# Kernel optimization log

Hardware: AMD Instinct MI355X
Metric: run time of the kernel (lower is better)

## Reference

```python
import jax, jax.numpy as jnp
import numpy as np

NUM_NODES = 40000
NUM_EDGES = 400000
DIM = 128
NUM_REL = 502  # num_relation * 2
NUM_HEAD = 1


def setup_inputs() -> dict:
    key = jax.random.key(0)
    ks = jax.random.split(key, 16)
    d = DIM
    return {
        "curr_stat": jax.random.normal(ks[0], (NUM_NODES, d), jnp.float32),
        "last_stat": jax.random.normal(ks[1], (NUM_NODES, d), jnp.float32),
        "relemb_weight": jax.random.normal(ks[2], (NUM_REL, d), jnp.float32),
        "selfrel_weight": jax.random.normal(ks[3], (1, d), jnp.float32),
        "Wq": jax.random.normal(ks[4], (2 * d, d), jnp.float32) * (1.0 / np.sqrt(2 * d)),
        "bq": jax.random.normal(ks[5], (d,), jnp.float32) * 0.02,
        "Wk": jax.random.normal(ks[6], (2 * d, d), jnp.float32) * (1.0 / np.sqrt(2 * d)),
        "bk": jax.random.normal(ks[7], (d,), jnp.float32) * 0.02,
        "Wv": jax.random.normal(ks[8], (d, d), jnp.float32) * (1.0 / np.sqrt(d)),
        "bv": jax.random.normal(ks[9], (d,), jnp.float32) * 0.02,
        "dyn_weight": jax.random.normal(ks[10], (d, d), jnp.float32) * (1.0 / np.sqrt(d)),
        "edge_index": jax.random.randint(ks[11], (2, NUM_EDGES), 0, NUM_NODES, jnp.int32),
        "edge_type": jax.random.randint(ks[12], (NUM_EDGES,), 0, NUM_REL, jnp.int32),
    }


def _segment_softmax(scores, seg, num_segments):
    # scores: [E, H]; softmax over edges sharing the same destination segment
    m = jax.ops.segment_max(scores, seg, num_segments=num_segments)  # [N, H]
    e = jnp.exp(scores - m[seg])
    s = jax.ops.segment_sum(e, seg, num_segments=num_segments)  # [N, H]
    return e / s[seg]


def reference(curr_stat, last_stat, relemb_weight, selfrel_weight,
              Wq, bq, Wk, bk, Wv, bv, dyn_weight,
              edge_index, edge_type):
    N, D = curr_stat.shape
    H = NUM_HEAD
    HD = D // H

    # append self-loop edges for every node, with the dedicated self-relation
    loop = jnp.arange(N, dtype=edge_index.dtype)
    src = jnp.concatenate([edge_index[0], loop])  # [E_total]
    dst = jnp.concatenate([edge_index[1], loop])  # [E_total]
    type_emb = jnp.concatenate(
        [relemb_weight[edge_type], jnp.broadcast_to(selfrel_weight, (N, D))], axis=0)

    E = src.shape[0]
    # linear projections (x @ W + b); torch Linear stores W transposed, same math
    q = (jnp.concatenate([curr_stat[dst], type_emb], -1) @ Wq + bq).reshape(E, H, HD)
    k = (jnp.concatenate([last_stat[src], type_emb], -1) @ Wk + bk).reshape(E, H, HD)
    v = (last_stat[src] @ Wv + bv).reshape(E, H, HD)

    attn = jnp.sum(q * k, axis=-1) / np.sqrt(HD).astype(np.float32)  # [E, H]

    dyn_prob = _segment_softmax(attn, dst, N)   # [E, H]
    sta_prob = _segment_softmax(-attn, dst, N)  # [E, H]

    counts = jax.ops.segment_sum(jnp.ones((E,), jnp.float32), dst, num_segments=N)
    denom = jnp.maximum(counts, 1.0)[:, None]  # scatter-mean denominator

    feat_dyn = jax.ops.segment_sum((dyn_prob[..., None] * v).reshape(E, D), dst,
                                   num_segments=N) / denom
    feat_sta = jax.ops.segment_sum((sta_prob[..., None] * v).reshape(E, D), dst,
                                   num_segments=N) / denom

    # stack (feat_sta, feat_dyn @ dyn_weight) -> [2, N, D]
    return jnp.stack([feat_sta, feat_dyn @ dyn_weight])
```

## Files before the change

kernel.cpp:

```cpp
#include <hip/hip_runtime.h>
#include <hip/hip_bf16.h>
#include <math.h>

#define DIMC 128

typedef __attribute__((ext_vector_type(8))) short short8;
typedef __attribute__((ext_vector_type(4))) float floatx4;
typedef __attribute__((ext_vector_type(2))) float f32x2;

static __device__ __forceinline__ unsigned pk2(float lo, float hi) {
    __hip_bfloat162 h = __float22bfloat162_rn(make_float2(lo, hi));
    return *(unsigned*)&h;
}
static __device__ __forceinline__ unsigned short f2bf(float x) {
    union { float f; unsigned int u; } v; v.f = x;
    unsigned int r = v.u + 0x7FFFu + ((v.u >> 16) & 1u);
    return (unsigned short)(r >> 16);
}
static __device__ __forceinline__ f32x2 bfp(unsigned int u) {
    union { unsigned int i; float f; } a, b;
    a.i = u << 16; b.i = u & 0xFFFF0000u;
    f32x2 r; r.x = a.f; r.y = b.f; return r;
}

template<int CTRL>
static __device__ __forceinline__ float dpp_add(float x) {
    int y = __builtin_amdgcn_update_dpp(0, __float_as_int(x), CTRL, 0xF, 0xF, true);
    return x + __int_as_float(y);
}
static __device__ __forceinline__ float red32(float p) {
    p = dpp_add<0xB1>(p);
    p = dpp_add<0x4E>(p);
    p = dpp_add<0x141>(p);
    p = dpp_add<0x140>(p);
    p += __shfl_xor(p, 16);
    return p;
}

struct PrepArgs {
    const float* W[6];
    unsigned short* F[6];
    const float* relemb; const float* selfrel;
    float* TypeEmb;
    int* deg;
    int R; int N;
};

__global__ __launch_bounds__(64) void prep_all(PrepArgs a)
{
    int b = blockIdx.x;
    int lane = threadIdx.x;
    if (b < 192) {
        int mat = b >> 5, ts = b & 31;
        int s = ts & 3, t = ts >> 2;
        int q = lane >> 4, c = lane & 15;
        const float* W = a.W[mat];
        unsigned short o[8];
        #pragma unroll
        for (int j = 0; j < 8; ++j)
            o[j] = f2bf(W[(long)(s * 32 + q * 8 + j) * DIMC + t * 16 + c]);
        uint4 u;
        u.x = (unsigned)o[0] | ((unsigned)o[1] << 16);
        u.y = (unsigned)o[2] | ((unsigned)o[3] << 16);
        u.z = (unsigned)o[4] | ((unsigned)o[5] << 16);
        u.w = (unsigned)o[6] | ((unsigned)o[7] << 16);
        ((uint4*)a.F[mat])[ts * 64 + lane] = u;
    } else if (b < 192 + a.R + 1) {
        int r = b - 192;
        const float* src = (r < a.R) ? (a.relemb + (long)r * DIMC) : a.selfrel;
        float2 v = ((const float2*)src)[lane];
        ((float2*)(a.TypeEmb + (long)r * DIMC))[lane] = v;
    } else {
        int i = (b - (192 + a.R + 1)) * 64 + lane;
        if (i < a.N) a.deg[i] = 0;
    }
}

struct GemmM5 {
    const float*          Af[5];
    const unsigned short* Ab[5];
    const unsigned short* F[5];
    const float*          bias[5];
    float*                outf[5];
    unsigned short*       outb[5];
    int                   ostride[5];
    int                   ooff[5];
    int                   M[5];
    const int*            hist_dst;
    int*                  hist_deg;
    int                   hist_E;
};

__global__ __launch_bounds__(256) void gemm_mfma(GemmM5 g)
{
    if (blockIdx.y == 5) {
        int i = blockIdx.x * blockDim.x + threadIdx.x;
        int stride = gridDim.x * blockDim.x;
        for (; i < g.hist_E; i += stride) atomicAdd(&g.hist_deg[g.hist_dst[i]], 1);
        return;
    }

    const int which = blockIdx.y;
    const int M = g.M[which];
    if (blockIdx.x * 64 >= M) return;

    const float*          __restrict__ Af   = g.Af[which];
    const unsigned short* __restrict__ Ab   = g.Ab[which];
    const unsigned short* __restrict__ F    = g.F[which];
    const float*          __restrict__ bias = g.bias[which];
    float*          __restrict__ outf = g.outf[which];
    unsigned short* __restrict__ outb = g.outb[which];
    const int ostride = g.ostride[which];
    const int ooff    = g.ooff[which];

    const int wave = threadIdx.x >> 6;
    const int lane = threadIdx.x & 63;
    const int q = lane >> 4, c = lane & 15;
    const int rowbase = blockIdx.x * 64 + wave * 16;

    short8 wf[8][4];
    const uint4* Fp = (const uint4*)F;
    #pragma unroll
    for (int t = 0; t < 8; ++t)
        #pragma unroll
        for (int s = 0; s < 4; ++s) {
            uint4 u = Fp[(t * 4 + s) * 64 + lane];
            wf[t][s] = *(short8*)&u;
        }

    floatx4 acc[8];
    #pragma unroll
    for (int t = 0; t < 8; ++t) {
        float b = bias ? bias[t * 16 + c] : 0.0f;
        acc[t] = (floatx4){b, b, b, b};
    }

    int rowA = rowbase + c; if (rowA > M - 1) rowA = M - 1;
    short8 af[4];
    if (Af) {
        const float* Ar = Af + (long)rowA * DIMC + q * 8;
        #pragma unroll
        for (int s = 0; s < 4; ++s) {
            float4 x0 = *(const float4*)(Ar + s * 32);
            float4 x1 = *(const float4*)(Ar + s * 32 + 4);
            uint4 u;
            u.x = pk2(x0.x, x0.y);
            u.y = pk2(x0.z, x0.w);
            u.z = pk2(x1.x, x1.y);
            u.w = pk2(x1.z, x1.w);
            af[s] = *(short8*)&u;
        }
    } else {
        const unsigned short* Ar = Ab + (long)rowA * DIMC + q * 8;
        #pragma unroll
        for (int s = 0; s < 4; ++s) {
            uint4 u = *(const uint4*)(Ar + s * 32);
            af[s] = *(short8*)&u;
        }
    }

    #pragma unroll
    for (int t = 0; t < 8; ++t)
        #pragma unroll
        for (int s = 0; s < 4; ++s)
            acc[t] = __builtin_amdgcn_mfma_f32_16x16x32_bf16(af[s], wf[t][s], acc[t], 0, 0, 0);

    if (outf) {
        #pragma unroll
        for (int t = 0; t < 8; ++t)
            #pragma unroll
            for (int r = 0; r < 4; ++r) {
                int row = rowbase + q * 4 + r;
                if (row < M)
                    outf[(long)row * DIMC + t * 16 + c] = acc[t][r];
            }
    } else {
        #pragma unroll
        for (int t = 0; t < 8; ++t)
            #pragma unroll
            for (int r = 0; r < 4; ++r) {
                float other = __shfl_xor(acc[t][r], 1);
                int row = rowbase + q * 4 + r;
                if ((lane & 1) == 0 && row < M) {
                    unsigned word = pk2(acc[t][r], other);
                    ((unsigned*)outb)[((long)row * 64 + t * 8 + (c >> 1))
                                      * (long)ostride + ooff] = word;
                }
            }
    }
}

__global__ __launch_bounds__(256) void partial_sums(const int* __restrict__ deg,
                                                    int* __restrict__ partial, int N)
{
    __shared__ int sh[256];
    int t = threadIdx.x;
    int beg = blockIdx.x * 1024 + t * 4;
    int s = 0;
    if (beg + 3 < N) { int4 v = *(const int4*)(deg + beg); s = v.x + v.y + v.z + v.w; }
    else { for (int j = 0; j < 4; ++j) if (beg + j < N) s += deg[beg + j]; }
    sh[t] = s;
    __syncthreads();
    for (int d = 128; d >= 1; d >>= 1) {
        if (t < d) sh[t] += sh[t + d];
        __syncthreads();
    }
    if (t == 0) partial[blockIdx.x] = sh[0];
}

__global__ __launch_bounds__(256) void scan_write_offsets(const int* __restrict__ deg,
                                                          const int* __restrict__ partial,
                                                          int* __restrict__ offs,
                                                          int* __restrict__ cursor, int N, int nb)
{
    __shared__ int sh[256];
    __shared__ int sbase;
    int t = threadIdx.x;
    if (t < 64) {
        int v = (t < nb && t < (int)blockIdx.x) ? partial[t] : 0;
        #pragma unroll
        for (int d = 32; d >= 1; d >>= 1) v += __shfl_xor(v, d);
        if (t == 0) sbase = v;
    }
    int beg = blockIdx.x * 1024 + t * 4;
    int d0 = 0, d1 = 0, d2 = 0, d3 = 0;
    if (beg + 3 < N) { int4 v = *(const int4*)(deg + beg); d0 = v.x; d1 = v.y; d2 = v.z; d3 = v.w; }
    else {
        if (beg < N)     d0 = deg[beg];
        if (beg + 1 < N) d1 = deg[beg + 1];
        if (beg + 2 < N) d2 = deg[beg + 2];
        if (beg + 3 < N) d3 = deg[beg + 3];
    }
    int s = d0 + d1 + d2 + d3;
    sh[t] = s;
    __syncthreads();
    for (int d = 1; d < 256; d <<= 1) {
        int v = (t >= d) ? sh[t - d] : 0;
        __syncthreads();
        sh[t] += v;
        __syncthreads();
    }
    int base = sbase + sh[t] - s;
    int o0 = base, o1 = o0 + d0, o2 = o1 + d1, o3 = o2 + d2;
    if (beg < N)     { offs[beg]     = o0; cursor[beg]     = o0; }
    if (beg + 1 < N) { offs[beg + 1] = o1; cursor[beg + 1] = o1; }
    if (beg + 2 < N) { offs[beg + 2] = o2; cursor[beg + 2] = o2; }
    if (beg + 3 < N) { offs[beg + 3] = o3; cursor[beg + 3] = o3; }
}

__global__ void scatter_kernel(const int* __restrict__ src, const int* __restrict__ dst,
                               const int* __restrict__ etype, int* __restrict__ cursor,
                               int2* __restrict__ sedge, int E)
{
    int e = blockIdx.x * blockDim.x + threadIdx.x;
    if (e < E) {
        int d = dst[e];
        int p = atomicAdd(&cursor[d], 1);
        sedge[p] = make_int2(src[e] << 8, etype[e] << 9);
    }
}

__global__ __launch_bounds__(256) void node_kernel(
    const float* __restrict__ Qn,
    const char*  __restrict__ Kb,
    const char*  __restrict__ Vb,
    const char*  __restrict__ QKb,
    const int* __restrict__ offs, const int* __restrict__ deg,
    const int2* __restrict__ sedge,
    float* __restrict__ out_sta, uint2* __restrict__ feat_dyn,
    int N, int R)
{
    int n = (blockIdx.x * blockDim.x + threadIdx.x) >> 6;
    int lane = threadIdx.x & 63;
    if (n >= N) return;
    const int hl = lane & 31;
    const int h  = lane >> 5;
    const int lo8  = hl << 3;
    const int lo16 = hl << 4;

    const float cs2 = 0.08838834764831845f * 1.4426950408889634f;
    int base = offs[n];
    int dcnt = deg[n];

    float4 qn4 = ((const float4*)(Qn + (long)n * DIMC))[hl];
    f32x2 q01; q01.x = qn4.x; q01.y = qn4.y;
    f32x2 q23; q23.x = qn4.z; q23.y = qn4.w;

    uint2 ks  = *(const uint2*)(Kb + ((long)n << 8) + lo8);
    uint2 vs  = *(const uint2*)(Vb + ((long)n << 8) + lo8);
    uint4 qks = *(const uint4*)(QKb + ((long)R << 9) + lo16);
    {
        f32x2 s0 = q01 + bfp(qks.x);
        f32x2 s1 = q23 + bfp(qks.z);
        f32x2 k0 = bfp(ks.x) + bfp(qks.y);
        f32x2 k1 = bfp(ks.y) + bfp(qks.w);
        f32x2 dp = s0 * k0;
        dp += s1 * k1;
        float p = red32(dp.x + dp.y);
        float t = p * cs2;
        float wd = (h == 0) ? exp2f(t)  : 0.0f;
        float ws = (h == 0) ? exp2f(-t) : 0.0f;
        f32x2 v0 = bfp(vs.x), v1 = bfp(vs.y);

        float s_d = wd, s_s = ws;
        f32x2 accd0 = v0 * wd, accd1 = v1 * wd;
        f32x2 accs0 = v0 * ws, accs1 = v1 * ws;

        int T = (dcnt + 3) >> 2;
        for (int it = 0; it < T; ++it) {
            int iA = 4 * it + 2 * h, iB = iA + 1;
            bool vA = iA < dcnt, vB = iB < dcnt;
            int2 eA = sedge[vA ? (base + iA) : 0];
            int2 eB = sedge[vB ? (base + iB) : 0];
            uint2 kA  = *(const uint2*)(Kb + eA.x + lo8);
            uint2 vAv = *(const uint2*)(Vb + eA.x + lo8);
            uint4 qkA = *(const uint4*)(QKb + eA.y + lo16);
            uint2 kB  = *(const uint2*)(Kb + eB.x + lo8);
            uint2 vBv = *(const uint2*)(Vb + eB.x + lo8);
            uint4 qkB = *(const uint4*)(QKb + eB.y + lo16);

            f32x2 a0 = q01 + bfp(qkA.x), a1 = q23 + bfp(qkA.z);
            f32x2 ka0 = bfp(kA.x) + bfp(qkA.y), ka1 = bfp(kA.y) + bfp(qkA.w);
            f32x2 da = a0 * ka0;
            da += a1 * ka1;
            float pA = da.x + da.y;

            f32x2 b0 = q01 + bfp(qkB.x), b1 = q23 + bfp(qkB.z);
            f32x2 kb0 = bfp(kB.x) + bfp(qkB.y), kb1 = bfp(kB.y) + bfp(qkB.w);
            f32x2 db = b0 * kb0;
            db += b1 * kb1;
            float pB = db.x + db.y;

            pA = red32(pA);
            pB = red32(pB);
            float tA = pA * cs2, tB = pB * cs2;

            float wdA = vA ? exp2f(tA)  : 0.0f;
            float wsA = vA ? exp2f(-tA) : 0.0f;
            float wdB = vB ? exp2f(tB)  : 0.0f;
            float wsB = vB ? exp2f(-tB) : 0.0f;

            s_d += wdA + wdB;
            s_s += wsA + wsB;

            f32x2 va0 = bfp(vAv.x), va1 = bfp(vAv.y);
            f32x2 vb0 = bfp(vBv.x), vb1 = bfp(vBv.y);
            accd0 += va0 * wdA;  accd0 += vb0 * wdB;
            accd1 += va1 * wdA;  accd1 += vb1 * wdB;
            accs0 += va0 * wsA;  accs0 += vb0 * wsB;
            accs1 += va1 * wsA;  accs1 += vb1 * wsB;
        }

        s_d += __shfl_xor(s_d, 32);
        s_s += __shfl_xor(s_s, 32);
        accd0.x += __shfl_xor(accd0.x, 32); accd0.y += __shfl_xor(accd0.y, 32);
        accd1.x += __shfl_xor(accd1.x, 32); accd1.y += __shfl_xor(accd1.y, 32);
        accs0.x += __shfl_xor(accs0.x, 32); accs0.y += __shfl_xor(accs0.y, 32);
        accs1.x += __shfl_xor(accs1.x, 32); accs1.y += __shfl_xor(accs1.y, 32);

        if (h == 0) {
            float denom = (float)(dcnt + 1);
            float id_ = 1.0f / (s_d * denom);
            float is_ = 1.0f / (s_s * denom);
            ((float4*)(out_sta + (long)n * DIMC))[hl] =
                make_float4(accs0.x * is_, accs0.y * is_, accs1.x * is_, accs1.y * is_);
            feat_dyn[(unsigned)n * 32u + hl] =
                make_uint2(pk2(accd0.x * id_, accd0.y * id_), pk2(accd1.x * id_, accd1.y * id_));
        }
    }
}

extern "C" void kernel_launch(void* const* d_in, const int* in_sizes, int n_in,
                              void* d_out, int out_size, void* d_ws, size_t ws_size,
                              hipStream_t stream)
{
    const float* curr    = (const float*)d_in[0];
    const float* last    = (const float*)d_in[1];
    const float* relemb  = (const float*)d_in[2];
    const float* selfrel = (const float*)d_in[3];
    const float* Wq      = (const float*)d_in[4];
    const float* bq      = (const float*)d_in[5];
    const float* Wk      = (const float*)d_in[6];
    const float* bk      = (const float*)d_in[7];
    const float* Wv      = (const float*)d_in[8];
    const float* bv      = (const float*)d_in[9];
    const float* dynw    = (const float*)d_in[10];
    const int*   eidx    = (const int*)d_in[11];
    const int*   etype   = (const int*)d_in[12];
    float* out = (float*)d_out;

    const int N = in_sizes[0] / DIMC;
    const int E = in_sizes[12];
    const int R = in_sizes[2] / DIMC;
    const int* esrc = eidx;
    const int* edst = eidx + E;

    char* wp = (char*)d_ws;
    auto alloc = [&](size_t bytes) { char* r = wp; wp += (bytes + 15) & ~(size_t)15; return r; };
    size_t nd = (size_t)N * DIMC;
    float*          Qn    = (float*)alloc(nd * 4);
    unsigned short* Kb    = (unsigned short*)alloc((size_t)N * 256);
    unsigned short* Vb    = (unsigned short*)alloc((size_t)N * 256);
    unsigned short* Fdb   = (unsigned short*)alloc(nd * 2);
    uint4*          QKre  = (uint4*)alloc((size_t)(R + 1) * 32 * 16);
    float*          TypeEmb = (float*)alloc((size_t)(R + 2) * DIMC * 4);
    unsigned short* FW[6];
    for (int m = 0; m < 6; ++m) FW[m] = (unsigned short*)alloc(2048 * 8 * 2);
    int*            deg   = (int*)alloc((size_t)N * 4);
    int*            offs  = (int*)alloc((size_t)N * 4);
    int*            cursor= (int*)alloc((size_t)N * 4);
    int2*           sedge = (int2*)alloc((size_t)E * 8);
    int*            partial = (int*)alloc(256 * 4);

    const int gblk = N / 64;
    const int sblk = (N + 1023) / 1024;

    PrepArgs pa;
    pa.W[0] = Wq;   pa.W[1] = Wk;   pa.W[2] = Wv;
    pa.W[3] = dynw; pa.W[4] = Wq + (size_t)DIMC * DIMC; pa.W[5] = Wk + (size_t)DIMC * DIMC;
    for (int m = 0; m < 6; ++m) pa.F[m] = FW[m];
    pa.relemb = relemb; pa.selfrel = selfrel; pa.TypeEmb = TypeEmb;
    pa.deg = deg; pa.R = R; pa.N = N;
    int pgrid = 192 + (R + 1) + (N + 63) / 64;
    hipLaunchKernelGGL(prep_all, dim3(pgrid), dim3(64), 0, stream, pa);

    GemmM5 g5;
    for (int s = 0; s < 5; ++s) { g5.Ab[s] = nullptr; g5.outf[s] = nullptr; g5.outb[s] = nullptr; }
    g5.Af[0] = curr;    g5.F[0] = FW[0]; g5.bias[0] = nullptr; g5.outf[0] = Qn;
    g5.ostride[0] = 1;  g5.ooff[0] = 0;  g5.M[0] = N;
    g5.Af[1] = last;    g5.F[1] = FW[1]; g5.bias[1] = nullptr; g5.outb[1] = Kb;
    g5.ostride[1] = 1;  g5.ooff[1] = 0;  g5.M[1] = N;
    g5.Af[2] = last;    g5.F[2] = FW[2]; g5.bias[2] = bv;      g5.outb[2] = Vb;
    g5.ostride[2] = 1;  g5.ooff[2] = 0;  g5.M[2] = N;
    g5.Af[3] = TypeEmb; g5.F[3] = FW[4]; g5.bias[3] = bq;      g5.outb[3] = (unsigned short*)QKre;
    g5.ostride[3] = 2;  g5.ooff[3] = 0;  g5.M[3] = R + 1;
    g5.Af[4] = TypeEmb; g5.F[4] = FW[5]; g5.bias[4] = bk;      g5.outb[4] = (unsigned short*)QKre;
    g5.ostride[4] = 2;  g5.ooff[4] = 1;  g5.M[4] = R + 1;
    g5.hist_dst = edst; g5.hist_deg = deg; g5.hist_E = E;
    hipLaunchKernelGGL(gemm_mfma, dim3(gblk, 6), dim3(256), 0, stream, g5);

    hipLaunchKernelGGL(partial_sums, dim3(sblk), dim3(256), 0, stream, deg, partial, N);
    hipLaunchKernelGGL(scan_write_offsets, dim3(sblk), dim3(256), 0, stream,
                       deg, partial, offs, cursor, N, sblk);
    hipLaunchKernelGGL(scatter_kernel, dim3((E + 255) / 256), dim3(256), 0, stream,
                       esrc, edst, etype, cursor, sedge, E);

    hipLaunchKernelGGL(node_kernel, dim3((N + 3) / 4), dim3(256), 0, stream,
                       Qn, (const char*)Kb, (const char*)Vb, (const char*)QKre,
                       offs, deg, sedge, out, (uint2*)Fdb, N, R);

    GemmM5 gf;
    for (int s = 0; s < 5; ++s) { gf.Af[s] = nullptr; gf.Ab[s] = nullptr; gf.outf[s] = nullptr; gf.outb[s] = nullptr; gf.M[s] = 0; }
    gf.Ab[0] = Fdb; gf.F[0] = FW[3]; gf.bias[0] = nullptr; gf.outf[0] = out + nd;
    gf.ostride[0] = 1; gf.ooff[0] = 0; gf.M[0] = N;
    gf.hist_dst = edst; gf.hist_deg = deg; gf.hist_E = 0;
    hipLaunchKernelGGL(gemm_mfma, dim3(gblk, 1), dim3(256), 0, stream, gf);
}
```

Before: 221.3 us.

## Software-pipeline edge gathers in node kernel and fold softmax scale into Q weights

The node kernel's edge loop is restructured into a two-stage software pipeline: edge indices for the next iteration and K/V/QK gathers for the current one are issued before the compute on the previous batch, which hides gather latency. The attention scale (1/sqrt(D)·log2e) is folded into the Wq weights and the q-side bias during prep, removing per-edge multiplies. The block size drops from 256 to 128 threads (2 nodes per block). The cost is higher register pressure from the double-buffered loads and bf16 rounding applied to scaled weights.

```diff
diff --git a/kernel.cpp b/kernel.cpp
--- a/kernel.cpp
+++ b/kernel.cpp
@@ -3,6 +3,7 @@
 #include <math.h>
 
 #define DIMC 128
+#define CS2L (0.08838834764831845f * 1.4426950408889634f)
 
 typedef __attribute__((ext_vector_type(8))) short short8;
 typedef __attribute__((ext_vector_type(4))) float floatx4;
@@ -40,6 +41,7 @@
 struct PrepArgs {
     const float* W[6];
     unsigned short* F[6];
+    float wscale[6];
     const float* relemb; const float* selfrel;
     float* TypeEmb;
     int* deg;
@@ -55,10 +57,11 @@
         int s = ts & 3, t = ts >> 2;
         int q = lane >> 4, c = lane & 15;
         const float* W = a.W[mat];
+        float sc = a.wscale[mat];
         unsigned short o[8];
         #pragma unroll
         for (int j = 0; j < 8; ++j)
-            o[j] = f2bf(W[(long)(s * 32 + q * 8 + j) * DIMC + t * 16 + c]);
+            o[j] = f2bf(W[(long)(s * 32 + q * 8 + j) * DIMC + t * 16 + c] * sc);
         uint4 u;
         u.x = (unsigned)o[0] | ((unsigned)o[1] << 16);
         u.y = (unsigned)o[2] | ((unsigned)o[3] << 16);
@@ -81,6 +84,7 @@
     const unsigned short* Ab[5];
     const unsigned short* F[5];
     const float*          bias[5];
+    float                 bscale[5];
     float*                outf[5];
     unsigned short*       outb[5];
     int                   ostride[5];
@@ -108,6 +112,7 @@
     const unsigned short* __restrict__ Ab   = g.Ab[which];
     const unsigned short* __restrict__ F    = g.F[which];
     const float*          __restrict__ bias = g.bias[which];
+    const float bsc = g.bscale[which];
     float*          __restrict__ outf = g.outf[which];
     unsigned short* __restrict__ outb = g.outb[which];
     const int ostride = g.ostride[which];
@@ -131,7 +136,7 @@
     floatx4 acc[8];
     #pragma unroll
     for (int t = 0; t < 8; ++t) {
-        float b = bias ? bias[t * 16 + c] : 0.0f;
+        float b = bias ? bias[t * 16 + c] * bsc : 0.0f;
         acc[t] = (floatx4){b, b, b, b};
     }
 
@@ -260,7 +265,7 @@
     }
 }
 
-__global__ __launch_bounds__(256) void node_kernel(
+__global__ __launch_bounds__(128) void node_kernel(
     const float* __restrict__ Qn,
     const char*  __restrict__ Kb,
     const char*  __restrict__ Vb,
@@ -270,7 +275,7 @@
     float* __restrict__ out_sta, uint2* __restrict__ feat_dyn,
     int N, int R)
 {
-    int n = (blockIdx.x * blockDim.x + threadIdx.x) >> 6;
+    int n = blockIdx.x * 2 + (threadIdx.x >> 6);
     int lane = threadIdx.x & 63;
     if (n >= N) return;
     const int hl = lane & 31;
@@ -278,7 +283,6 @@
     const int lo8  = hl << 3;
     const int lo16 = hl << 4;
 
-    const float cs2 = 0.08838834764831845f * 1.4426950408889634f;
     int base = offs[n];
     int dcnt = deg[n];
 
@@ -289,6 +293,9 @@
     uint2 ks  = *(const uint2*)(Kb + ((long)n << 8) + lo8);
     uint2 vs  = *(const uint2*)(Vb + ((long)n << 8) + lo8);
     uint4 qks = *(const uint4*)(QKb + ((long)R << 9) + lo16);
+
+    float s_d, s_s;
+    f32x2 accd0, accd1, accs0, accs1;
     {
         f32x2 s0 = q01 + bfp(qks.x);
         f32x2 s1 = q23 + bfp(qks.z);
@@ -296,77 +303,102 @@
         f32x2 k1 = bfp(ks.y) + bfp(qks.w);
         f32x2 dp = s0 * k0;
         dp += s1 * k1;
-        float p = red32(dp.x + dp.y);
-        float t = p * cs2;
+        float t = red32(dp.x + dp.y);
         float wd = (h == 0) ? exp2f(t)  : 0.0f;
         float ws = (h == 0) ? exp2f(-t) : 0.0f;
         f32x2 v0 = bfp(vs.x), v1 = bfp(vs.y);
-
-        float s_d = wd, s_s = ws;
-        f32x2 accd0 = v0 * wd, accd1 = v1 * wd;
-        f32x2 accs0 = v0 * ws, accs1 = v1 * ws;
-
-        int T = (dcnt + 3) >> 2;
-        for (int it = 0; it < T; ++it) {
-            int iA = 4 * it + 2 * h, iB = iA + 1;
-            bool vA = iA < dcnt, vB = iB < dcnt;
-            int2 eA = sedge[vA ? (base + iA) : 0];
-            int2 eB = sedge[vB ? (base + iB) : 0];
-            uint2 kA  = *(const uint2*)(Kb + eA.x + lo8);
-            uint2 vAv = *(const uint2*)(Vb + eA.x + lo8);
-            uint4 qkA = *(const uint4*)(QKb + eA.y + lo16);
-            uint2 kB  = *(const uint2*)(Kb + eB.x + lo8);
-            uint2 vBv = *(const uint2*)(Vb + eB.x + lo8);
-            uint4 qkB = *(const uint4*)(QKb + eB.y + lo16);
-
-            f32x2 a0 = q01 + bfp(qkA.x), a1 = q23 + bfp(qkA.z);
-            f32x2 ka0 = bfp(kA.x) + bfp(qkA.y), ka1 = bfp(kA.y) + bfp(qkA.w);
-            f32x2 da = a0 * ka0;
-            da += a1 * ka1;
-            float pA = da.x + da.y;
-
-            f32x2 b0 = q01 + bfp(qkB.x), b1 = q23 + bfp(qkB.z);
-            f32x2 kb0 = bfp(kB.x) + bfp(qkB.y), kb1 = bfp(kB.y) + bfp(qkB.w);
-            f32x2 db = b0 * kb0;
-            db += b1 * kb1;
-            float pB = db.x + db.y;
-
-            pA = red32(pA);
-            pB = red32(pB);
-            float tA = pA * cs2, tB = pB * cs2;
-
-            float wdA = vA ? exp2f(tA)  : 0.0f;
-            float wsA = vA ? exp2f(-tA) : 0.0f;
-            float wdB = vB ? exp2f(tB)  : 0.0f;
-            float wsB = vB ? exp2f(-tB) : 0.0f;
-
-            s_d += wdA + wdB;
-            s_s += wsA + wsB;
-
-            f32x2 va0 = bfp(vAv.x), va1 = bfp(vAv.y);
-            f32x2 vb0 = bfp(vBv.x), vb1 = bfp(vBv.y);
-            accd0 += va0 * wdA;  accd0 += vb0 * wdB;
-            accd1 += va1 * wdA;  accd1 += vb1 * wdB;
-            accs0 += va0 * wsA;  accs0 += vb0 * wsB;
-            accs1 += va1 * wsA;  accs1 += vb1 * wsB;
+        s_d = wd; s_s = ws;
+        accd0 = v0 * wd; accd1 = v1 * wd;
+        accs0 = v0 * ws; accs1 = v1 * ws;
+    }
+
+    auto compute = [&](const uint2& kA, const uint2& vAv, const uint4& qkA,
+                       const uint2& kB, const uint2& vBv, const uint4& qkB, int it) {
+        int iA = 4 * it + 2 * h;
+        bool vA = iA < dcnt, vB = (iA + 1) < dcnt;
+
+        f32x2 a0 = q01 + bfp(qkA.x), a1 = q23 + bfp(qkA.z);
+        f32x2 ka0 = bfp(kA.x) + bfp(qkA.y), ka1 = bfp(kA.y) + bfp(qkA.w);
+        f32x2 da = a0 * ka0;
+        da += a1 * ka1;
+        float pA = da.x + da.y;
+
+        f32x2 b0 = q01 + bfp(qkB.x), b1 = q23 + bfp(qkB.z);
+        f32x2 kb0 = bfp(kB.x) + bfp(qkB.y), kb1 = bfp(kB.y) + bfp(qkB.w);
+        f32x2 db = b0 * kb0;
+        db += b1 * kb1;
+        float pB = db.x + db.y;
+
+        pA = red32(pA);
+        pB = red32(pB);
+
+        float wdA = vA ? exp2f(pA)  : 0.0f;
+        float wsA = vA ? exp2f(-pA) : 0.0f;
+        float wdB = vB ? exp2f(pB)  : 0.0f;
+        float wsB = vB ? exp2f(-pB) : 0.0f;
+
+        s_d += wdA + wdB;
+        s_s += wsA + wsB;
+
+        f32x2 va0 = bfp(vAv.x), va1 = bfp(vAv.y);
+        f32x2 vb0 = bfp(vBv.x), vb1 = bfp(vBv.y);
+        accd0 += va0 * wdA;  accd0 += vb0 * wdB;
+        accd1 += va1 * wdA;  accd1 += vb1 * wdB;
+        accs0 += va0 * wsA;  accs0 += vb0 * wsB;
+        accs1 += va1 * wsA;  accs1 += vb1 * wsB;
+    };
+
+    int T = (dcnt + 3) >> 2;
+    if (T > 0) {
+        int2 e0A, e0B, e1A, e1B;
+        uint2 g0kA, g0vA, g0kB, g0vB;  uint4 g0qA, g0qB;
+        uint2 g1kA, g1vA, g1kB, g1vB;  uint4 g1qA, g1qB;
+
+        #define LDE(it, ea, eb) { int iA_ = 4*(it) + 2*h; \
+            bool a_ = iA_ < dcnt, b_ = (iA_+1) < dcnt; \
+            ea = sedge[a_ ? base + iA_ : 0]; eb = sedge[b_ ? base + iA_ + 1 : 0]; }
+        #define LDG(ea, eb, kA_, vA_, qA_, kB_, vB_, qB_) { \
+            kA_ = *(const uint2*)(Kb + ea.x + lo8);  vA_ = *(const uint2*)(Vb + ea.x + lo8); \
+            qA_ = *(const uint4*)(QKb + ea.y + lo16); \
+            kB_ = *(const uint2*)(Kb + eb.x + lo8);  vB_ = *(const uint2*)(Vb + eb.x + lo8); \
+            qB_ = *(const uint4*)(QKb + eb.y + lo16); }
+
+        LDE(0, e0A, e0B);
+        LDG(e0A, e0B, g0kA, g0vA, g0qA, g0kB, g0vB, g0qB);
+        if (T > 1) LDE(1, e1A, e1B);
+
+        int it = 0;
+        for (;;) {
+            if (it + 1 >= T) { compute(g0kA, g0vA, g0qA, g0kB, g0vB, g0qB, it); break; }
+            LDG(e1A, e1B, g1kA, g1vA, g1qA, g1kB, g1vB, g1qB);
+            if (it + 2 < T) LDE(it + 2, e0A, e0B);
+            compute(g0kA, g0vA, g0qA, g0kB, g0vB, g0qB, it);
+            ++it;
+            if (it + 1 >= T) { compute(g1kA, g1vA, g1qA, g1kB, g1vB, g1qB, it); break; }
+            LDG(e0A, e0B, g0kA, g0vA, g0qA, g0kB, g0vB, g0qB);
+            if (it + 2 < T) LDE(it + 2, e1A, e1B);
+            compute(g1kA, g1vA, g1qA, g1kB, g1vB, g1qB, it);
+            ++it;
         }
-
-        s_d += __shfl_xor(s_d, 32);
-        s_s += __shfl_xor(s_s, 32);
-        accd0.x += __shfl_xor(accd0.x, 32); accd0.y += __shfl_xor(accd0.y, 32);
-        accd1.x += __shfl_xor(accd1.x, 32); accd1.y += __shfl_xor(accd1.y, 32);
-        accs0.x += __shfl_xor(accs0.x, 32); accs0.y += __shfl_xor(accs0.y, 32);
-        accs1.x += __shfl_xor(accs1.x, 32); accs1.y += __shfl_xor(accs1.y, 32);
-
-        if (h == 0) {
-            float denom = (float)(dcnt + 1);
-            float id_ = 1.0f / (s_d * denom);
-            float is_ = 1.0f / (s_s * denom);
-            ((float4*)(out_sta + (long)n * DIMC))[hl] =
-                make_float4(accs0.x * is_, accs0.y * is_, accs1.x * is_, accs1.y * is_);
-            feat_dyn[(unsigned)n * 32u + hl] =
-                make_uint2(pk2(accd0.x * id_, accd0.y * id_), pk2(accd1.x * id_, accd1.y * id_));
-        }
+        #undef LDE
+        #undef LDG
+    }
+
+    s_d += __shfl_xor(s_d, 32);
+    s_s += __shfl_xor(s_s, 32);
+    accd0.x += __shfl_xor(accd0.x, 32); accd0.y += __shfl_xor(accd0.y, 32);
+    accd1.x += __shfl_xor(accd1.x, 32); accd1.y += __shfl_xor(accd1.y, 32);
+    accs0.x += __shfl_xor(accs0.x, 32); accs0.y += __shfl_xor(accs0.y, 32);
+    accs1.x += __shfl_xor(accs1.x, 32); accs1.y += __shfl_xor(accs1.y, 32);
+
+    if (h == 0) {
+        float denom = (float)(dcnt + 1);
+        float id_ = 1.0f / (s_d * denom);
+        float is_ = 1.0f / (s_s * denom);
+        ((float4*)(out_sta + (long)n * DIMC))[hl] =
+            make_float4(accs0.x * is_, accs0.y * is_, accs1.x * is_, accs1.y * is_);
+        feat_dyn[(unsigned)n * 32u + hl] =
+            make_uint2(pk2(accd0.x * id_, accd0.y * id_), pk2(accd1.x * id_, accd1.y * id_));
     }
 }
 
@@ -418,6 +450,8 @@
     PrepArgs pa;
     pa.W[0] = Wq;   pa.W[1] = Wk;   pa.W[2] = Wv;
     pa.W[3] = dynw; pa.W[4] = Wq + (size_t)DIMC * DIMC; pa.W[5] = Wk + (size_t)DIMC * DIMC;
+    pa.wscale[0] = CS2L; pa.wscale[1] = 1.0f; pa.wscale[2] = 1.0f;
+    pa.wscale[3] = 1.0f; pa.wscale[4] = CS2L; pa.wscale[5] = 1.0f;
     for (int m = 0; m < 6; ++m) pa.F[m] = FW[m];
     pa.relemb = relemb; pa.selfrel = selfrel; pa.TypeEmb = TypeEmb;
     pa.deg = deg; pa.R = R; pa.N = N;
@@ -425,7 +459,7 @@
     hipLaunchKernelGGL(prep_all, dim3(pgrid), dim3(64), 0, stream, pa);
 
     GemmM5 g5;
-    for (int s = 0; s < 5; ++s) { g5.Ab[s] = nullptr; g5.outf[s] = nullptr; g5.outb[s] = nullptr; }
+    for (int s = 0; s < 5; ++s) { g5.Ab[s] = nullptr; g5.outf[s] = nullptr; g5.outb[s] = nullptr; g5.bscale[s] = 1.0f; }
     g5.Af[0] = curr;    g5.F[0] = FW[0]; g5.bias[0] = nullptr; g5.outf[0] = Qn;
     g5.ostride[0] = 1;  g5.ooff[0] = 0;  g5.M[0] = N;
     g5.Af[1] = last;    g5.F[1] = FW[1]; g5.bias[1] = nullptr; g5.outb[1] = Kb;
@@ -433,7 +467,7 @@
     g5.Af[2] = last;    g5.F[2] = FW[2]; g5.bias[2] = bv;      g5.outb[2] = Vb;
     g5.ostride[2] = 1;  g5.ooff[2] = 0;  g5.M[2] = N;
     g5.Af[3] = TypeEmb; g5.F[3] = FW[4]; g5.bias[3] = bq;      g5.outb[3] = (unsigned short*)QKre;
-    g5.ostride[3] = 2;  g5.ooff[3] = 0;  g5.M[3] = R + 1;
+    g5.ostride[3] = 2;  g5.ooff[3] = 0;  g5.M[3] = R + 1;      g5.bscale[3] = CS2L;
     g5.Af[4] = TypeEmb; g5.F[4] = FW[5]; g5.bias[4] = bk;      g5.outb[4] = (unsigned short*)QKre;
     g5.ostride[4] = 2;  g5.ooff[4] = 1;  g5.M[4] = R + 1;
     g5.hist_dst = edst; g5.hist_deg = deg; g5.hist_E = E;
@@ -445,12 +479,12 @@
     hipLaunchKernelGGL(scatter_kernel, dim3((E + 255) / 256), dim3(256), 0, stream,
                        esrc, edst, etype, cursor, sedge, E);
 
-    hipLaunchKernelGGL(node_kernel, dim3((N + 3) / 4), dim3(256), 0, stream,
+    hipLaunchKernelGGL(node_kernel, dim3((N + 1) / 2), dim3(128), 0, stream,
                        Qn, (const char*)Kb, (const char*)Vb, (const char*)QKre,
                        offs, deg, sedge, out, (uint2*)Fdb, N, R);
 
     GemmM5 gf;
-    for (int s = 0; s < 5; ++s) { gf.Af[s] = nullptr; gf.Ab[s] = nullptr; gf.outf[s] = nullptr; gf.outb[s] = nullptr; gf.M[s] = 0; }
+    for (int s = 0; s < 5; ++s) { gf.Af[s] = nullptr; gf.Ab[s] = nullptr; gf.outf[s] = nullptr; gf.outb[s] = nullptr; gf.M[s] = 0; gf.bscale[s] = 1.0f; }
     gf.Ab[0] = Fdb; gf.F[0] = FW[3]; gf.bias[0] = nullptr; gf.outf[0] = out + nd;
     gf.ostride[0] = 1; gf.ooff[0] = 0; gf.M[0] = N;
     gf.hist_dst = edst; gf.hist_deg = deg; gf.hist_E = 0;
```

Result: no change. 225.4 us (+1.9%).

## Process four edges per wave with 16-lane groups and fold softmax scale into weights

Applied to the files above, without the earlier changes.

The node kernel now splits each 64-lane wave into four 16-lane groups, each handling one edge with 8 features per lane, instead of two 32-lane halves handling two edges each. The self-loop is folded into the edge loop as a synthetic edge, and the dot-product reduction drops the cross-row shuffle. The 1/sqrt(d)*log2(e) score scale is pre-multiplied into the Q projection weights and relation-Q bias, which removes a multiply per edge. The cost is more shuffle-based merging across the four groups at the end, plus extra per-lane registers for accumulators.

```diff
diff --git a/kernel.cpp b/kernel.cpp
--- a/kernel.cpp
+++ b/kernel.cpp
@@ -3,6 +3,7 @@
 #include <math.h>
 
 #define DIMC 128
+#define CS2L (0.08838834764831845f * 1.4426950408889634f)
 
 typedef __attribute__((ext_vector_type(8))) short short8;
 typedef __attribute__((ext_vector_type(4))) float floatx4;
@@ -28,18 +29,18 @@
     int y = __builtin_amdgcn_update_dpp(0, __float_as_int(x), CTRL, 0xF, 0xF, true);
     return x + __int_as_float(y);
 }
-static __device__ __forceinline__ float red32(float p) {
+static __device__ __forceinline__ float red16(float p) {
     p = dpp_add<0xB1>(p);
     p = dpp_add<0x4E>(p);
     p = dpp_add<0x141>(p);
     p = dpp_add<0x140>(p);
-    p += __shfl_xor(p, 16);
     return p;
 }
 
 struct PrepArgs {
     const float* W[6];
     unsigned short* F[6];
+    float wscale[6];
     const float* relemb; const float* selfrel;
     float* TypeEmb;
     int* deg;
@@ -55,10 +56,11 @@
         int s = ts & 3, t = ts >> 2;
         int q = lane >> 4, c = lane & 15;
         const float* W = a.W[mat];
+        float sc = a.wscale[mat];
         unsigned short o[8];
         #pragma unroll
         for (int j = 0; j < 8; ++j)
-            o[j] = f2bf(W[(long)(s * 32 + q * 8 + j) * DIMC + t * 16 + c]);
+            o[j] = f2bf(W[(long)(s * 32 + q * 8 + j) * DIMC + t * 16 + c] * sc);
         uint4 u;
         u.x = (unsigned)o[0] | ((unsigned)o[1] << 16);
         u.y = (unsigned)o[2] | ((unsigned)o[3] << 16);
@@ -81,6 +83,7 @@
     const unsigned short* Ab[5];
     const unsigned short* F[5];
     const float*          bias[5];
+    float                 bscale[5];
     float*                outf[5];
     unsigned short*       outb[5];
     int                   ostride[5];
@@ -108,6 +111,7 @@
     const unsigned short* __restrict__ Ab   = g.Ab[which];
     const unsigned short* __restrict__ F    = g.F[which];
     const float*          __restrict__ bias = g.bias[which];
+    const float bsc = g.bscale[which];
     float*          __restrict__ outf = g.outf[which];
     unsigned short* __restrict__ outb = g.outb[which];
     const int ostride = g.ostride[which];
@@ -131,7 +135,7 @@
     floatx4 acc[8];
     #pragma unroll
     for (int t = 0; t < 8; ++t) {
-        float b = bias ? bias[t * 16 + c] : 0.0f;
+        float b = bias ? bias[t * 16 + c] * bsc : 0.0f;
         acc[t] = (floatx4){b, b, b, b};
     }
 
@@ -267,106 +271,86 @@
     const char*  __restrict__ QKb,
     const int* __restrict__ offs, const int* __restrict__ deg,
     const int2* __restrict__ sedge,
-    float* __restrict__ out_sta, uint2* __restrict__ feat_dyn,
+    float* __restrict__ out_sta, uint4* __restrict__ feat_dyn,
     int N, int R)
 {
     int n = (blockIdx.x * blockDim.x + threadIdx.x) >> 6;
     int lane = threadIdx.x & 63;
     if (n >= N) return;
-    const int hl = lane & 31;
-    const int h  = lane >> 5;
-    const int lo8  = hl << 3;
-    const int lo16 = hl << 4;
-
-    const float cs2 = 0.08838834764831845f * 1.4426950408889634f;
+    const int ql = lane & 15;
+    const int qt = lane >> 4;
+    const int lo16 = ql << 4;
+    const int lo32 = ql << 5;
+
     int base = offs[n];
     int dcnt = deg[n];
-
-    float4 qn4 = ((const float4*)(Qn + (long)n * DIMC))[hl];
-    f32x2 q01; q01.x = qn4.x; q01.y = qn4.y;
-    f32x2 q23; q23.x = qn4.z; q23.y = qn4.w;
-
-    uint2 ks  = *(const uint2*)(Kb + ((long)n << 8) + lo8);
-    uint2 vs  = *(const uint2*)(Vb + ((long)n << 8) + lo8);
-    uint4 qks = *(const uint4*)(QKb + ((long)R << 9) + lo16);
-    {
-        f32x2 s0 = q01 + bfp(qks.x);
-        f32x2 s1 = q23 + bfp(qks.z);
-        f32x2 k0 = bfp(ks.x) + bfp(qks.y);
-        f32x2 k1 = bfp(ks.y) + bfp(qks.w);
-        f32x2 dp = s0 * k0;
-        dp += s1 * k1;
-        float p = red32(dp.x + dp.y);
-        float t = p * cs2;
-        float wd = (h == 0) ? exp2f(t)  : 0.0f;
-        float ws = (h == 0) ? exp2f(-t) : 0.0f;
-        f32x2 v0 = bfp(vs.x), v1 = bfp(vs.y);
-
-        float s_d = wd, s_s = ws;
-        f32x2 accd0 = v0 * wd, accd1 = v1 * wd;
-        f32x2 accs0 = v0 * ws, accs1 = v1 * ws;
-
-        int T = (dcnt + 3) >> 2;
-        for (int it = 0; it < T; ++it) {
-            int iA = 4 * it + 2 * h, iB = iA + 1;
-            bool vA = iA < dcnt, vB = iB < dcnt;
-            int2 eA = sedge[vA ? (base + iA) : 0];
-            int2 eB = sedge[vB ? (base + iB) : 0];
-            uint2 kA  = *(const uint2*)(Kb + eA.x + lo8);
-            uint2 vAv = *(const uint2*)(Vb + eA.x + lo8);
-            uint4 qkA = *(const uint4*)(QKb + eA.y + lo16);
-            uint2 kB  = *(const uint2*)(Kb + eB.x + lo8);
-            uint2 vBv = *(const uint2*)(Vb + eB.x + lo8);
-            uint4 qkB = *(const uint4*)(QKb + eB.y + lo16);
-
-            f32x2 a0 = q01 + bfp(qkA.x), a1 = q23 + bfp(qkA.z);
-            f32x2 ka0 = bfp(kA.x) + bfp(qkA.y), ka1 = bfp(kA.y) + bfp(qkA.w);
-            f32x2 da = a0 * ka0;
-            da += a1 * ka1;
-            float pA = da.x + da.y;
-
-            f32x2 b0 = q01 + bfp(qkB.x), b1 = q23 + bfp(qkB.z);
-            f32x2 kb0 = bfp(kB.x) + bfp(qkB.y), kb1 = bfp(kB.y) + bfp(qkB.w);
-            f32x2 db = b0 * kb0;
-            db += b1 * kb1;
-            float pB = db.x + db.y;
-
-            pA = red32(pA);
-            pB = red32(pB);
-            float tA = pA * cs2, tB = pB * cs2;
-
-            float wdA = vA ? exp2f(tA)  : 0.0f;
-            float wsA = vA ? exp2f(-tA) : 0.0f;
-            float wdB = vB ? exp2f(tB)  : 0.0f;
-            float wsB = vB ? exp2f(-tB) : 0.0f;
-
-            s_d += wdA + wdB;
-            s_s += wsA + wsB;
-
-            f32x2 va0 = bfp(vAv.x), va1 = bfp(vAv.y);
-            f32x2 vb0 = bfp(vBv.x), vb1 = bfp(vBv.y);
-            accd0 += va0 * wdA;  accd0 += vb0 * wdB;
-            accd1 += va1 * wdA;  accd1 += vb1 * wdB;
-            accs0 += va0 * wsA;  accs0 += vb0 * wsB;
-            accs1 += va1 * wsA;  accs1 += vb1 * wsB;
-        }
-
-        s_d += __shfl_xor(s_d, 32);
-        s_s += __shfl_xor(s_s, 32);
-        accd0.x += __shfl_xor(accd0.x, 32); accd0.y += __shfl_xor(accd0.y, 32);
-        accd1.x += __shfl_xor(accd1.x, 32); accd1.y += __shfl_xor(accd1.y, 32);
-        accs0.x += __shfl_xor(accs0.x, 32); accs0.y += __shfl_xor(accs0.y, 32);
-        accs1.x += __shfl_xor(accs1.x, 32); accs1.y += __shfl_xor(accs1.y, 32);
-
-        if (h == 0) {
-            float denom = (float)(dcnt + 1);
-            float id_ = 1.0f / (s_d * denom);
-            float is_ = 1.0f / (s_s * denom);
-            ((float4*)(out_sta + (long)n * DIMC))[hl] =
-                make_float4(accs0.x * is_, accs0.y * is_, accs1.x * is_, accs1.y * is_);
-            feat_dyn[(unsigned)n * 32u + hl] =
-                make_uint2(pk2(accd0.x * id_, accd0.y * id_), pk2(accd1.x * id_, accd1.y * id_));
-        }
+    int etot = dcnt + 1;
+
+    const float4* qp = (const float4*)(Qn + (long)n * DIMC + ql * 8);
+    float4 qa = qp[0], qb = qp[1];
+    f32x2 q01; q01.x = qa.x; q01.y = qa.y;
+    f32x2 q23; q23.x = qa.z; q23.y = qa.w;
+    f32x2 q45; q45.x = qb.x; q45.y = qb.y;
+    f32x2 q67; q67.x = qb.z; q67.y = qb.w;
+
+    float s_d = 0.0f, s_s = 0.0f;
+    f32x2 accd0 = {0.f, 0.f}, accd1 = accd0, accd2 = accd0, accd3 = accd0;
+    f32x2 accs0 = accd0, accs1 = accd0, accs2 = accd0, accs3 = accd0;
+
+    const int selfK = n << 8, selfQ = R << 9;
+
+    int T = (etot + 3) >> 2;
+    for (int it = 0; it < T; ++it) {
+        int i = 4 * it + qt;
+        bool vv = i < etot;
+        bool re = i < dcnt;
+        int2 e = re ? sedge[base + i] : make_int2(selfK, selfQ);
+
+        uint4 kx  = *(const uint4*)(Kb + e.x + lo16);
+        uint4 vx  = *(const uint4*)(Vb + e.x + lo16);
+        uint4 qk0 = *(const uint4*)(QKb + e.y + lo32);
+        uint4 qk1 = *(const uint4*)(QKb + e.y + lo32 + 16);
+
+        f32x2 a0 = q01 + bfp(qk0.x), a1 = q23 + bfp(qk0.z);
+        f32x2 a2 = q45 + bfp(qk1.x), a3 = q67 + bfp(qk1.z);
+        f32x2 k0 = bfp(kx.x) + bfp(qk0.y), k1 = bfp(kx.y) + bfp(qk0.w);
+        f32x2 k2 = bfp(kx.z) + bfp(qk1.y), k3 = bfp(kx.w) + bfp(qk1.w);
+        f32x2 dp = a0 * k0;
+        dp += a1 * k1;
+        dp += a2 * k2;
+        dp += a3 * k3;
+        float p = red16(dp.x + dp.y);
+
+        float wd = vv ? exp2f(p)  : 0.0f;
+        float ws = vv ? exp2f(-p) : 0.0f;
+        s_d += wd; s_s += ws;
+
+        f32x2 v0 = bfp(vx.x), v1 = bfp(vx.y), v2 = bfp(vx.z), v3 = bfp(vx.w);
+        accd0 += v0 * wd; accd1 += v1 * wd; accd2 += v2 * wd; accd3 += v3 * wd;
+        accs0 += v0 * ws; accs1 += v1 * ws; accs2 += v2 * ws; accs3 += v3 * ws;
+    }
+
+    #define MRG(x) { x += __shfl_xor(x, 16); x += __shfl_xor(x, 32); }
+    MRG(s_d) MRG(s_s)
+    MRG(accd0.x) MRG(accd0.y) MRG(accd1.x) MRG(accd1.y)
+    MRG(accd2.x) MRG(accd2.y) MRG(accd3.x) MRG(accd3.y)
+    MRG(accs0.x) MRG(accs0.y) MRG(accs1.x) MRG(accs1.y)
+    MRG(accs2.x) MRG(accs2.y) MRG(accs3.x) MRG(accs3.y)
+    #undef MRG
+
+    if (qt == 0) {
+        float denom = (float)(dcnt + 1);
+        float id_ = 1.0f / (s_d * denom);
+        float is_ = 1.0f / (s_s * denom);
+        float4* op = (float4*)(out_sta + (long)n * DIMC + ql * 8);
+        op[0] = make_float4(accs0.x * is_, accs0.y * is_, accs1.x * is_, accs1.y * is_);
+        op[1] = make_float4(accs2.x * is_, accs2.y * is_, accs3.x * is_, accs3.y * is_);
+        uint4 w;
+        w.x = pk2(accd0.x * id_, accd0.y * id_);
+        w.y = pk2(accd1.x * id_, accd1.y * id_);
+        w.z = pk2(accd2.x * id_, accd2.y * id_);
+        w.w = pk2(accd3.x * id_, accd3.y * id_);
+        feat_dyn[(unsigned)n * 16u + ql] = w;
     }
 }
 
@@ -418,6 +402,8 @@
     PrepArgs pa;
     pa.W[0] = Wq;   pa.W[1] = Wk;   pa.W[2] = Wv;
     pa.W[3] = dynw; pa.W[4] = Wq + (size_t)DIMC * DIMC; pa.W[5] = Wk + (size_t)DIMC * DIMC;
+    pa.wscale[0] = CS2L; pa.wscale[1] = 1.0f; pa.wscale[2] = 1.0f;
+    pa.wscale[3] = 1.0f; pa.wscale[4] = CS2L; pa.wscale[5] = 1.0f;
     for (int m = 0; m < 6; ++m) pa.F[m] = FW[m];
     pa.relemb = relemb; pa.selfrel = selfrel; pa.TypeEmb = TypeEmb;
     pa.deg = deg; pa.R = R; pa.N = N;
@@ -425,7 +411,7 @@
     hipLaunchKernelGGL(prep_all, dim3(pgrid), dim3(64), 0, stream, pa);
 
     GemmM5 g5;
-    for (int s = 0; s < 5; ++s) { g5.Ab[s] = nullptr; g5.outf[s] = nullptr; g5.outb[s] = nullptr; }
+    for (int s = 0; s < 5; ++s) { g5.Ab[s] = nullptr; g5.outf[s] = nullptr; g5.outb[s] = nullptr; g5.bscale[s] = 1.0f; }
     g5.Af[0] = curr;    g5.F[0] = FW[0]; g5.bias[0] = nullptr; g5.outf[0] = Qn;
     g5.ostride[0] = 1;  g5.ooff[0] = 0;  g5.M[0] = N;
     g5.Af[1] = last;    g5.F[1] = FW[1]; g5.bias[1] = nullptr; g5.outb[1] = Kb;
@@ -433,7 +419,7 @@
     g5.Af[2] = last;    g5.F[2] = FW[2]; g5.bias[2] = bv;      g5.outb[2] = Vb;
     g5.ostride[2] = 1;  g5.ooff[2] = 0;  g5.M[2] = N;
     g5.Af[3] = TypeEmb; g5.F[3] = FW[4]; g5.bias[3] = bq;      g5.outb[3] = (unsigned short*)QKre;
-    g5.ostride[3] = 2;  g5.ooff[3] = 0;  g5.M[3] = R + 1;
+    g5.ostride[3] = 2;  g5.ooff[3] = 0;  g5.M[3] = R + 1;      g5.bscale[3] = CS2L;
     g5.Af[4] = TypeEmb; g5.F[4] = FW[5]; g5.bias[4] = bk;      g5.outb[4] = (unsigned short*)QKre;
     g5.ostride[4] = 2;  g5.ooff[4] = 1;  g5.M[4] = R + 1;
     g5.hist_dst = edst; g5.hist_deg = deg; g5.hist_E = E;
@@ -447,10 +433,10 @@
 
     hipLaunchKernelGGL(node_kernel, dim3((N + 3) / 4), dim3(256), 0, stream,
                        Qn, (const char*)Kb, (const char*)Vb, (const char*)QKre,
-                       offs, deg, sedge, out, (uint2*)Fdb, N, R);
+                       offs, deg, sedge, out, (uint4*)Fdb, N, R);
 
     GemmM5 gf;
-    for (int s = 0; s < 5; ++s) { gf.Af[s] = nullptr; gf.Ab[s] = nullptr; gf.outf[s] = nullptr; gf.outb[s] = nullptr; gf.M[s] = 0; }
+    for (int s = 0; s < 5; ++s) { gf.Af[s] = nullptr; gf.Ab[s] = nullptr; gf.outf[s] = nullptr; gf.outb[s] = nullptr; gf.M[s] = 0; gf.bscale[s] = 1.0f; }
     gf.Ab[0] = Fdb; gf.F[0] = FW[3]; gf.bias[0] = nullptr; gf.outf[0] = out + nd;
     gf.ostride[0] = 1; gf.ooff[0] = 0; gf.M[0] = N;
     gf.hist_dst = edst; gf.hist_deg = deg; gf.hist_E = 0;
```

Measured after the change: 224.7 us. No clear change (+1.6%).
